# Performance work log

Measured on AMD Instinct MI355X. Metric: run time of the kernel, lower is better.

Reference implementation:

```python
import jax, jax.numpy as jnp
import numpy as np


def _l2norm(x, eps=1e-6):
    # Matches F.normalize(p=2, dim=-1, eps=eps): divide by max(||x||, eps)
    n = jnp.sqrt(jnp.sum(x * x, axis=-1, keepdims=True))
    return x / jnp.maximum(n, eps)


def setup_inputs() -> dict:
    key = jax.random.key(0)
    k0, k1, k2, k3, k4 = jax.random.split(key, 5)
    B, T, H, Dk, Dv = 2, 4096, 16, 128, 128
    q = _l2norm(jax.random.normal(k0, (B, T, H, Dk), dtype=jnp.float32))
    k = _l2norm(jax.random.normal(k1, (B, T, H, Dk), dtype=jnp.float32))
    v = jax.random.normal(k2, (B, T, H, Dv), dtype=jnp.float32)
    # alpha: decay in (0,1) (module: exp(-exp(A_log)*softplus(a+dt_bias)))
    alpha = jax.random.uniform(k3, (B, T, H), dtype=jnp.float32, minval=0.5, maxval=0.999)
    # beta: write gate in (0,1) (module: sigmoid(b))
    beta = jax.random.uniform(k4, (B, T, H), dtype=jnp.float32, minval=0.01, maxval=0.99)
    initial_state = jnp.zeros((B, H, Dk, Dv), dtype=jnp.float32)
    return {"q": q, "k": k, "v": v, "alpha": alpha, "beta": beta,
            "initial_state": initial_state}


def reference(q, k, v, alpha, beta, initial_state):
    """Gated delta rule recurrence (faithful to gdn_recurrent_naive).

    S_t = a_t * (S_{t-1} - b_t * k_t (k_t^T S_{t-1})) + b_t * k_t v_t^T
    o_t = S_t^T q_t
    """
    def step(S, xs):
        q_t, k_t, v_t, a_t, b_t = xs  # (B,H,Dk), (B,H,Dk), (B,H,Dv), (B,H), (B,H)
        a = a_t[..., None, None]
        b = b_t[..., None, None]
        kS = jnp.einsum('bhd,bhdv->bhv', k_t, S)          # k^T S
        S = a * (S - b * jnp.einsum('bhd,bhv->bhdv', k_t, kS)) \
            + b * jnp.einsum('bhd,bhv->bhdv', k_t, v_t)   # delta-rule update
        o = jnp.einsum('bhdv,bhd->bhv', S, q_t)           # read with q
        return S, o

    xs = (q.swapaxes(0, 1), k.swapaxes(0, 1), v.swapaxes(0, 1),
          alpha.swapaxes(0, 1), beta.swapaxes(0, 1))  # time-major for scan
    S_final, outs = jax.lax.scan(step, initial_state.astype(jnp.float32), xs)
    return outs.swapaxes(0, 1), S_final  # (B,T,H,Dv), (B,H,Dk,Dv)
```

## Files before the change

### kernel.cpp

```cpp
#include <hip/hip_runtime.h>

#define T_LEN 4096
#define H_N   16
#define DK    128
#define DV    128
#define LCH   64
#define NCH   64

typedef float f32x4 __attribute__((ext_vector_type(4)));
typedef short s16x8 __attribute__((ext_vector_type(8)));

#define OFF_U0 0
#define OFF_W  32768
#define OFF_Q  49152
#define OFF_KD 65536
#define OFF_G  81920
#define OFF_GM 90112
#define CH_B   90368ull
#define WS_NEED (2048ull * CH_B)

#define SWZ(row) (((row)&7) << 4)

__device__ __forceinline__ unsigned short f2b(float x) {
  unsigned u = __float_as_uint(x);
  return (unsigned short)((u + 0x7FFF + ((u >> 16) & 1)) >> 16);
}

#define GLDS16(gp, lp)                                                        \
  __builtin_amdgcn_global_load_lds(                                           \
      (const __attribute__((address_space(1))) void*)(gp),                    \
      (__attribute__((address_space(3))) void*)(lp), 16, 0, 0)
#define GLDS4(gp, lp)                                                         \
  __builtin_amdgcn_global_load_lds(                                           \
      (const __attribute__((address_space(1))) void*)(gp),                    \
      (__attribute__((address_space(3))) void*)(lp), 4, 0, 0)

#define LBAR()                                                                \
  do {                                                                        \
    asm volatile("s_waitcnt lgkmcnt(0)" ::: "memory");                        \
    __builtin_amdgcn_s_barrier();                                             \
    __builtin_amdgcn_sched_barrier(0);                                        \
  } while (0)

__device__ void solve64(float* RHS, const float* A, int tid) {
#pragma unroll 1
  for (int I = 0; I < 4; ++I) {
    if (I > 0) {
      const int i2 = 16 * I + (tid >> 4), cg = tid & 15;
      float* rp = RHS + i2 * 128 + cg * 8;
      float acc[8];
#pragma unroll
      for (int m = 0; m < 8; ++m) acc[m] = rp[m];
      for (int j = 0; j < 16 * I; ++j) {
        float a = A[i2 * 64 + j];
        const float* yp = RHS + j * 128 + cg * 8;
#pragma unroll
        for (int m = 0; m < 8; ++m) acc[m] = fmaf(-a, yp[m], acc[m]);
      }
#pragma unroll
      for (int m = 0; m < 8; ++m) rp[m] = acc[m];
      __syncthreads();
    }
    if (tid < 128) {
      const int col = tid;
      float y[16];
#pragma unroll
      for (int r = 0; r < 16; ++r) y[r] = RHS[(16 * I + r) * 128 + col];
#pragma unroll
      for (int r = 1; r < 16; ++r) {
        float t = y[r];
#pragma unroll
        for (int j = 0; j < 15; ++j)
          if (j < r) t = fmaf(-A[(16 * I + r) * 64 + 16 * I + j], y[j], t);
        y[r] = t;
      }
#pragma unroll
      for (int r = 0; r < 16; ++r) RHS[(16 * I + r) * 128 + col] = y[r];
    }
    __syncthreads();
  }
}

extern "C" __global__ void __launch_bounds__(256) gdn_p1(
    const float* __restrict__ q, const float* __restrict__ k,
    const float* __restrict__ v, const float* __restrict__ al,
    const float* __restrict__ be, char* __restrict__ ws) {
  __shared__ unsigned char big[32768];
  __shared__ float A_s[64 * 64];
  __shared__ float g_s[64], bb_s[64], sc_s[64];
  unsigned char* Kb = big;
  unsigned char* Qb = big + 16384;
  float* RHS = (float*)big;

  const int bid = blockIdx.x;
  const int bh = bid & 31, c = bid >> 5;
  const int b = bh >> 4, h = bh & 15;
  const int tid = threadIdx.x;
  const int t0 = c * LCH;
  char* wsc = ws + (size_t)(bh * 64 + c) * CH_B;

  if (tid < 64) {
    size_t gi = (size_t)(b * T_LEN + t0 + tid) * H_N + h;
    g_s[tid] = __logf(al[gi]);
    bb_s[tid] = be[gi];
  }
  __syncthreads();
  if (tid == 0) {
    float r = 0.f;
    for (int i = 0; i < 64; ++i) { r += g_s[i]; g_s[i] = r; }
  }
  __syncthreads();
  if (tid < 64) {
    sc_s[tid] = __expf(g_s[tid]);
    *(float*)(wsc + OFF_GM + tid * 4) = sc_s[tid];
  }

  for (int idx = tid; idx < 1024; idx += 256) {
    int row = idx >> 4, grp = idx & 15;
    size_t go = ((size_t)(b * T_LEN + t0 + row) * H_N + h) * DK + grp * 8;
    float4 ka = *(const float4*)(k + go);
    float4 kb2 = *(const float4*)(k + go + 4);
    float4 qa = *(const float4*)(q + go);
    float4 qb2 = *(const float4*)(q + go + 4);
    union { unsigned short u[8]; uint4 v4; } tk, tq;
    tk.u[0] = f2b(ka.x); tk.u[1] = f2b(ka.y); tk.u[2] = f2b(ka.z); tk.u[3] = f2b(ka.w);
    tk.u[4] = f2b(kb2.x); tk.u[5] = f2b(kb2.y); tk.u[6] = f2b(kb2.z); tk.u[7] = f2b(kb2.w);
    tq.u[0] = f2b(qa.x); tq.u[1] = f2b(qa.y); tq.u[2] = f2b(qa.z); tq.u[3] = f2b(qa.w);
    tq.u[4] = f2b(qb2.x); tq.u[5] = f2b(qb2.y); tq.u[6] = f2b(qb2.z); tq.u[7] = f2b(qb2.w);
    int la = (row * 256 + grp * 16) ^ SWZ(row);
    *(uint4*)(Kb + la) = tk.v4;
    *(uint4*)(Qb + la) = tq.v4;
    *(uint4*)(wsc + OFF_Q + la) = tq.v4;
  }
  __syncthreads();

  const int w = tid >> 6, l = tid & 63, li = l & 15, hi = l >> 4;
  f32x4 aK[4], aQ[4];
#pragma unroll
  for (int jt = 0; jt < 4; ++jt) { aK[jt] = (f32x4){0, 0, 0, 0}; aQ[jt] = (f32x4){0, 0, 0, 0}; }
#pragma unroll
  for (int ks = 0; ks < 4; ++ks) {
    int rowA = 16 * w + li;
    int oa = (rowA * 256 + ks * 64 + hi * 16) ^ SWZ(rowA);
    s16x8 fa = *(const s16x8*)(Kb + oa);
    s16x8 fq = *(const s16x8*)(Qb + oa);
#pragma unroll
    for (int jt = 0; jt < 4; ++jt) {
      int rowB = 16 * jt + li;
      s16x8 fb = *(const s16x8*)(Kb + ((rowB * 256 + ks * 64 + hi * 16) ^ SWZ(rowB)));
      aK[jt] = __builtin_amdgcn_mfma_f32_16x16x32_bf16(fa, fb, aK[jt], 0, 0, 0);
      aQ[jt] = __builtin_amdgcn_mfma_f32_16x16x32_bf16(fq, fb, aQ[jt], 0, 0, 0);
    }
  }
#pragma unroll
  for (int jt = 0; jt < 4; ++jt)
#pragma unroll
    for (int r = 0; r < 4; ++r) {
      int i = 16 * w + hi * 4 + r, j = 16 * jt + li;
      float e = __expf(g_s[i] - g_s[j]);
      A_s[i * 64 + j] = (j < i) ? bb_s[i] * e * aK[jt][r] : 0.f;
      *(unsigned short*)(wsc + OFF_G + ((i * 128 + j * 2) ^ SWZ(i))) =
          f2b((j <= i) ? e * aQ[jt][r] : 0.f);
    }
  __syncthreads();

  for (int idx = tid; idx < 2048; idx += 256) {
    int row = idx >> 5, c4 = idx & 31;
    float4 vv = *(const float4*)(v + ((size_t)(b * T_LEN + t0 + row) * H_N + h) * DV + c4 * 4);
    float s = bb_s[row];
    float4 o = {s * vv.x, s * vv.y, s * vv.z, s * vv.w};
    *(float4*)(RHS + row * 128 + c4 * 4) = o;
  }
  __syncthreads();
  solve64(RHS, A_s, tid);
  for (int idx = tid; idx < 2048; idx += 256) {
    int row = idx >> 5, c4 = idx & 31;
    *(float4*)(wsc + OFF_U0 + (c4 >> 2) * 4096 + row * 64 + (c4 & 3) * 16) =
        *(const float4*)(RHS + idx * 4);
  }
  __syncthreads();

  for (int idx = tid; idx < 2048; idx += 256) {
    int row = idx >> 5, c4 = idx & 31;
    float4 kv = *(const float4*)(k + ((size_t)(b * T_LEN + t0 + row) * H_N + h) * DK + c4 * 4);
    float s = bb_s[row] * sc_s[row];
    float4 o = {s * kv.x, s * kv.y, s * kv.z, s * kv.w};
    *(float4*)(RHS + row * 128 + c4 * 4) = o;
  }
  __syncthreads();
  solve64(RHS, A_s, tid);
  for (int idx = tid; idx < 1024; idx += 256) {
    int row = idx >> 4, g8 = idx & 15;
    const float* p = RHS + row * 128 + g8 * 8;
    union { unsigned short u[8]; uint4 v4; } t;
#pragma unroll
    for (int e = 0; e < 8; ++e) t.u[e] = f2b(-p[e]);
    *(uint4*)(wsc + OFF_W + ((row * 256 + g8 * 16) ^ SWZ(row))) = t.v4;
  }
  __syncthreads();

  if (tid < 64) sc_s[tid] = __expf(g_s[63] - g_s[tid]);
  __syncthreads();
  float* Kf = (float*)big;
#pragma unroll 1
  for (int p = 0; p < 2; ++p) {
    for (int idx = tid; idx < 1024; idx += 256) {
      int r = idx >> 5, c4 = idx & 31;
      float4 kv = *(const float4*)(k + ((size_t)(b * T_LEN + t0 + 32 * p + r) * H_N + h) * DK + c4 * 4);
      *(float4*)(Kf + r * 132 + c4 * 4) = kv;
    }
    __syncthreads();
#pragma unroll
    for (int m = 0; m < 16; ++m) {
      int flat = m * 256 + tid;
      int j32 = flat & 31, d = flat >> 5;
      float val = sc_s[32 * p + j32] * Kf[j32 * 132 + d];
      *(unsigned short*)(wsc + OFF_KD + ((d * 128 + (32 * p + j32) * 2) ^ SWZ(d))) = f2b(val);
    }
    __syncthreads();
  }
}

extern "C" __global__ void __launch_bounds__(256, 1) gdn_p2(
    const float* __restrict__ S0, float* __restrict__ out,
    const char* __restrict__ ws) {
  __shared__ unsigned char Wb[2][16384];
  __shared__ unsigned char Qb[2][16384];
  __shared__ unsigned char KDb[2][16384];
  __shared__ unsigned char Gb[2][8192];
  __shared__ float U0s[2][1024];
  __shared__ float gam[2][64];
  __shared__ unsigned char Stb[4096];
  __shared__ unsigned char Ytb[2048];

  const int bid = blockIdx.x;
  const int bh = bid & 31, s = bid >> 5;
  const int b = bh >> 4, h = bh & 15;
  const int tid = threadIdx.x;
  const int w = tid >> 6, lane = tid & 63, li = lane & 15, hi = lane >> 4;
  const char* wsbase = ws + (size_t)bh * 64 * CH_B;

#define STG(CI, P)                                                            \
  do {                                                                        \
    const char* c_ = wsbase + (size_t)(CI) * CH_B;                            \
    _Pragma("unroll") for (int j_ = 0; j_ < 4; ++j_) {                        \
      GLDS16(c_ + OFF_W + j_ * 4096 + tid * 16, &Wb[P][j_ * 4096 + w * 1024]); \
      GLDS16(c_ + OFF_Q + j_ * 4096 + tid * 16, &Qb[P][j_ * 4096 + w * 1024]); \
      GLDS16(c_ + OFF_KD + j_ * 4096 + tid * 16, &KDb[P][j_ * 4096 + w * 1024]); \
    }                                                                         \
    _Pragma("unroll") for (int j_ = 0; j_ < 2; ++j_)                          \
      GLDS16(c_ + OFF_G + j_ * 4096 + tid * 16, &Gb[P][j_ * 4096 + w * 1024]); \
    GLDS16(c_ + OFF_U0 + s * 4096 + tid * 16,                                 \
           (unsigned char*)U0s[P] + w * 1024);                                \
    if (w == 0) GLDS4(c_ + OFF_GM + lane * 4, &gam[P][0]);                    \
  } while (0)

  float S[2][4];
#pragma unroll
  for (int t = 0; t < 2; ++t)
#pragma unroll
    for (int r = 0; r < 4; ++r) {
      int d = (w + 4 * t) * 16 + hi * 4 + r;
      S[t][r] = S0[((size_t)bh * 128 + d) * 128 + s * 16 + li];
    }
#define WRITE_ST()                                                            \
  do {                                                                        \
    _Pragma("unroll") for (int t = 0; t < 2; ++t)                             \
        _Pragma("unroll") for (int r = 0; r < 4; r += 2) {                    \
      int d = (w + 4 * t) * 16 + hi * 4 + r;                                  \
      unsigned pk = (unsigned)f2b(S[t][r]) | ((unsigned)f2b(S[t][r + 1]) << 16); \
      *(unsigned*)(Stb + ((li * 256 + d * 2) ^ SWZ(li))) = pk;                \
    }                                                                         \
  } while (0)

  STG(0, 0);
  WRITE_ST();
  __syncthreads();

#pragma unroll 1
  for (int c = 0; c < NCH; ++c) {
    const int p = c & 1;
    if (c + 1 < NCH) STG(c + 1, p ^ 1);

    s16x8 sfb[4];
#pragma unroll
    for (int ks = 0; ks < 4; ++ks)
      sfb[ks] = *(const s16x8*)(Stb + ((li * 256 + ks * 64 + hi * 16) ^ SWZ(li)));

    f32x4 Y;
#pragma unroll
    for (int r = 0; r < 4; ++r) Y[r] = U0s[p][(16 * w + hi * 4 + r) * 16 + li];
#pragma unroll
    for (int ks = 0; ks < 4; ++ks) {
      s16x8 fa = *(const s16x8*)(Wb[p] + (((16 * w + li) * 256 + ks * 64 + hi * 16) ^ SWZ(li)));
      Y = __builtin_amdgcn_mfma_f32_16x16x32_bf16(fa, sfb[ks], Y, 0, 0, 0);
    }
#pragma unroll
    for (int r = 0; r < 4; r += 2) {
      int j = 16 * w + hi * 4 + r;
      unsigned pk = (unsigned)f2b(Y[r]) | ((unsigned)f2b(Y[r + 1]) << 16);
      *(unsigned*)(Ytb + ((li * 128 + j * 2) ^ SWZ(li))) = pk;
    }
    LBAR();

    f32x4 O = {0, 0, 0, 0};
#pragma unroll
    for (int ks = 0; ks < 4; ++ks) {
      s16x8 fa = *(const s16x8*)(Qb[p] + (((16 * w + li) * 256 + ks * 64 + hi * 16) ^ SWZ(li)));
      O = __builtin_amdgcn_mfma_f32_16x16x32_bf16(fa, sfb[ks], O, 0, 0, 0);
    }
    s16x8 yfb[2];
#pragma unroll
    for (int ks = 0; ks < 2; ++ks)
      yfb[ks] = *(const s16x8*)(Ytb + ((li * 128 + ks * 64 + hi * 16) ^ SWZ(li)));
#pragma unroll
    for (int r = 0; r < 4; ++r) O[r] *= gam[p][16 * w + hi * 4 + r];
#pragma unroll
    for (int ks = 0; ks < 2; ++ks) {
      s16x8 fa = *(const s16x8*)(Gb[p] + (((16 * w + li) * 128 + ks * 64 + hi * 16) ^ SWZ(li)));
      O = __builtin_amdgcn_mfma_f32_16x16x32_bf16(fa, yfb[ks], O, 0, 0, 0);
    }
#pragma unroll
    for (int r = 0; r < 4; ++r) {
      size_t oi = ((size_t)(b * T_LEN + c * 64 + 16 * w + hi * 4 + r) * H_N + h) * DV + s * 16 + li;
      out[oi] = O[r];
    }

    float ge = gam[p][63];
#pragma unroll
    for (int t = 0; t < 2; ++t) {
      f32x4 acc;
#pragma unroll
      for (int r = 0; r < 4; ++r) acc[r] = ge * S[t][r];
#pragma unroll
      for (int ks = 0; ks < 2; ++ks) {
        s16x8 fa = *(const s16x8*)(KDb[p] + ((((w + 4 * t) * 16 + li) * 128 + ks * 64 + hi * 16) ^ SWZ(li)));
        acc = __builtin_amdgcn_mfma_f32_16x16x32_bf16(fa, yfb[ks], acc, 0, 0, 0);
      }
#pragma unroll
      for (int r = 0; r < 4; ++r) S[t][r] = acc[r];
    }
    LBAR();
    WRITE_ST();
    __syncthreads();
  }

#pragma unroll
  for (int t = 0; t < 2; ++t)
#pragma unroll
    for (int r = 0; r < 4; ++r) {
      int d = (w + 4 * t) * 16 + hi * 4 + r;
      out[(size_t)(2 * T_LEN * H_N * DV) + ((size_t)bh * 128 + d) * 128 + s * 16 + li] = S[t][r];
    }
}

#define COLS 16
#define CHUNK 16
#define STEP_B 8192u
#define AB_B 64u
#define OSTRIDE (H_N * DV)
template <int CTRL>
__device__ __forceinline__ float dpp_add(float x) {
  int y = __builtin_amdgcn_update_dpp(0, __float_as_int(x), CTRL, 0xF, 0xF, true);
  return x + __int_as_float(y);
}
__device__ __forceinline__ float red16(float x) {
  x = dpp_add<0xB1>(x); x = dpp_add<0x4E>(x);
  x = dpp_add<0x124>(x); x = dpp_add<0x128>(x);
  return x;
}
extern "C" __global__ void __launch_bounds__(256, 1) gdn_fallback(
    const float* __restrict__ q, const float* __restrict__ k,
    const float* __restrict__ v, const float* __restrict__ al,
    const float* __restrict__ be, const float* __restrict__ S0,
    float* __restrict__ out) {
  __shared__ float kb[2][CHUNK * DK];
  __shared__ float qb[2][CHUNK * DK];
  __shared__ float vb[2][CHUNK * COLS];
  __shared__ float abuf[2][64];
  __shared__ float bbuf[2][64];
  const int bid = blockIdx.x;
  const int bh = bid & 31, g = bid >> 5;
  const int b = bh >> 4, h = bh & 15;
  const int tid = threadIdx.x;
  const int cl = tid >> 4, li = tid & 15, lane = tid & 63, wid = tid >> 6;
  const int col = g * COLS + cl, d0 = li * 8;
  const size_t bh_qk = ((size_t)b * T_LEN * H_N + h) * DK;
  const size_t bh_v = ((size_t)b * T_LEN * H_N + h) * DV;
  const size_t bh_ab = (size_t)b * T_LEN * H_N + h;
  const int fo0 = wid * 2048 + lane * 16, fo1 = fo0 + 1024;
  const char* kg0 = (const char*)(k + bh_qk) + (size_t)(fo0 >> 9) * STEP_B + (fo0 & 511);
  const char* kg1 = (const char*)(k + bh_qk) + (size_t)(fo1 >> 9) * STEP_B + (fo1 & 511);
  const char* qg0 = (const char*)(q + bh_qk) + (size_t)(fo0 >> 9) * STEP_B + (fo0 & 511);
  const char* qg1 = (const char*)(q + bh_qk) + (size_t)(fo1 >> 9) * STEP_B + (fo1 & 511);
  const int fv = lane * 16;
  const char* vg = (const char*)(v + bh_v + g * COLS) + (size_t)(fv >> 6) * STEP_B + (fv & 63);
  const int lcl = lane < 16 ? lane : 15;
  const char* ag = (const char*)(al + bh_ab) + (size_t)lcl * AB_B;
  const char* bg = (const char*)(be + bh_ab) + (size_t)lcl * AB_B;
#define STAGEF(CI, P) do { \
    const size_t off = (size_t)(CI) * (CHUNK * STEP_B); \
    const size_t offab = (size_t)(CI) * (CHUNK * AB_B); \
    GLDS16(kg0 + off, &kb[P][wid * 512]); GLDS16(kg1 + off, &kb[P][wid * 512 + 256]); \
    GLDS16(qg0 + off, &qb[P][wid * 512]); GLDS16(qg1 + off, &qb[P][wid * 512 + 256]); \
    if (wid == 0) GLDS16(vg + off, &vb[P][0]); \
    else if (wid == 1) GLDS4(ag + offab, &abuf[P][0]); \
    else if (wid == 2) GLDS4(bg + offab, &bbuf[P][0]); \
  } while (0)
  float sv[8];
  const float* s0p = S0 + ((size_t)(b * H_N + h) * DK + d0) * DV + col;
#pragma unroll
  for (int j = 0; j < 8; ++j) sv[j] = s0p[(size_t)j * DV];
  STAGEF(0, 0);
  __syncthreads();
  float* op = out + bh_v + col;
  for (int ci = 0; ci < T_LEN / CHUNK; ++ci) {
    const int p = ci & 1;
    if (ci + 1 < T_LEN / CHUNK) STAGEF(ci + 1, p ^ 1);
    const float* kc = kb[p]; const float* qc = qb[p]; const float* vc = vb[p];
    const float* ac = abuf[p]; const float* bc = bbuf[p];
#pragma unroll
    for (int j = 0; j < CHUNK; ++j) {
      f32x4 kA = *(const f32x4*)(kc + j * DK + d0);
      f32x4 kB = *(const f32x4*)(kc + j * DK + d0 + 4);
      f32x4 qA = *(const f32x4*)(qc + j * DK + d0);
      f32x4 qB = *(const f32x4*)(qc + j * DK + d0 + 4);
      float vv = vc[j * COLS + cl], aa = ac[j], bv = bc[j];
      float kk[8] = {kA[0], kA[1], kA[2], kA[3], kB[0], kB[1], kB[2], kB[3]};
      float qq[8] = {qA[0], qA[1], qA[2], qA[3], qB[0], qB[1], qB[2], qB[3]};
      float pk0 = kk[0] * sv[0], pk1 = kk[1] * sv[1];
      float pu0 = qq[0] * sv[0], pu1 = qq[1] * sv[1];
      float pg0 = kk[0] * qq[0], pg1 = kk[1] * qq[1];
#pragma unroll
      for (int m = 2; m < 8; m += 2) {
        pk0 = fmaf(kk[m], sv[m], pk0); pk1 = fmaf(kk[m + 1], sv[m + 1], pk1);
        pu0 = fmaf(qq[m], sv[m], pu0); pu1 = fmaf(qq[m + 1], sv[m + 1], pu1);
        pg0 = fmaf(kk[m], qq[m], pg0); pg1 = fmaf(kk[m + 1], qq[m + 1], pg1);
      }
      float pk = red16(pk0 + pk1), pu = red16(pu0 + pu1), pg = red16(pg0 + pg1);
      float tmp = fmaf(-(bv * aa), pk, bv * vv);
#pragma unroll
      for (int m = 0; m < 8; ++m) sv[m] = fmaf(aa, sv[m], kk[m] * tmp);
      if (li == 0) op[(size_t)(ci * CHUNK + j) * OSTRIDE] = fmaf(pg, tmp, aa * pu);
    }
    __syncthreads();
  }
  float* sf = out + (size_t)2 * T_LEN * H_N * DV + ((size_t)(b * H_N + h) * DK + d0) * DV + col;
#pragma unroll
  for (int j = 0; j < 8; ++j) sf[(size_t)j * DV] = sv[j];
}

extern "C" void kernel_launch(void* const* d_in, const int* in_sizes, int n_in,
                              void* d_out, int out_size, void* d_ws,
                              size_t ws_size, hipStream_t stream) {
  const float* q = (const float*)d_in[0];
  const float* k = (const float*)d_in[1];
  const float* v = (const float*)d_in[2];
  const float* al = (const float*)d_in[3];
  const float* be = (const float*)d_in[4];
  const float* S0 = (const float*)d_in[5];
  float* out = (float*)d_out;

  if (ws_size >= WS_NEED) {
    gdn_p1<<<dim3(2048), dim3(256), 0, stream>>>(q, k, v, al, be, (char*)d_ws);
    gdn_p2<<<dim3(256), dim3(256), 0, stream>>>(S0, out, (const char*)d_ws);
  } else {
    gdn_fallback<<<dim3(256), dim3(256), 0, stream>>>(q, k, v, al, be, S0, out);
  }
}
```

Measured before the change: 296.6 us.

## Solve both triangular systems per-thread in registers, fuse KD write, parallel prefix scan

Replaces the two shared-memory blocked triangular solves with a single register-resident forward substitution. Threads 0-127 each solve one column of the V right-hand side and threads 128-255 each solve one column of the K right-hand side concurrently, with A rows read as float4 from LDS. The serial single-thread cumulative log-decay sum becomes a wavefront shuffle scan, and the decayed-K transpose write is fused into the K load, dropping several barriers and LDS round trips. In exchange each thread holds 64 floats of state, which raises register pressure and may cause spills or lower occupancy, and global loads and stores become strided per column.

```diff
diff --git a/kernel.cpp b/kernel.cpp
--- a/kernel.cpp
+++ b/kernel.cpp
@@ -42,55 +42,15 @@
     __builtin_amdgcn_sched_barrier(0);                                        \
   } while (0)
 
-__device__ void solve64(float* RHS, const float* A, int tid) {
-#pragma unroll 1
-  for (int I = 0; I < 4; ++I) {
-    if (I > 0) {
-      const int i2 = 16 * I + (tid >> 4), cg = tid & 15;
-      float* rp = RHS + i2 * 128 + cg * 8;
-      float acc[8];
-#pragma unroll
-      for (int m = 0; m < 8; ++m) acc[m] = rp[m];
-      for (int j = 0; j < 16 * I; ++j) {
-        float a = A[i2 * 64 + j];
-        const float* yp = RHS + j * 128 + cg * 8;
-#pragma unroll
-        for (int m = 0; m < 8; ++m) acc[m] = fmaf(-a, yp[m], acc[m]);
-      }
-#pragma unroll
-      for (int m = 0; m < 8; ++m) rp[m] = acc[m];
-      __syncthreads();
-    }
-    if (tid < 128) {
-      const int col = tid;
-      float y[16];
-#pragma unroll
-      for (int r = 0; r < 16; ++r) y[r] = RHS[(16 * I + r) * 128 + col];
-#pragma unroll
-      for (int r = 1; r < 16; ++r) {
-        float t = y[r];
-#pragma unroll
-        for (int j = 0; j < 15; ++j)
-          if (j < r) t = fmaf(-A[(16 * I + r) * 64 + 16 * I + j], y[j], t);
-        y[r] = t;
-      }
-#pragma unroll
-      for (int r = 0; r < 16; ++r) RHS[(16 * I + r) * 128 + col] = y[r];
-    }
-    __syncthreads();
-  }
-}
-
 extern "C" __global__ void __launch_bounds__(256) gdn_p1(
     const float* __restrict__ q, const float* __restrict__ k,
     const float* __restrict__ v, const float* __restrict__ al,
     const float* __restrict__ be, char* __restrict__ ws) {
-  __shared__ unsigned char big[32768];
-  __shared__ float A_s[64 * 64];
-  __shared__ float g_s[64], bb_s[64], sc_s[64];
+  __shared__ __align__(16) unsigned char big[32768];
+  __shared__ __align__(16) float A_s[64 * 64];
+  __shared__ float g_s[64], bb_s[64], sc_s[64], rr_s[64], bg_s[64];
   unsigned char* Kb = big;
   unsigned char* Qb = big + 16384;
-  float* RHS = (float*)big;
 
   const int bid = blockIdx.x;
   const int bh = bid & 31, c = bid >> 5;
@@ -101,18 +61,21 @@
 
   if (tid < 64) {
     size_t gi = (size_t)(b * T_LEN + t0 + tid) * H_N + h;
-    g_s[tid] = __logf(al[gi]);
-    bb_s[tid] = be[gi];
-  }
-  __syncthreads();
-  if (tid == 0) {
-    float r = 0.f;
-    for (int i = 0; i < 64; ++i) { r += g_s[i]; g_s[i] = r; }
-  }
-  __syncthreads();
-  if (tid < 64) {
-    sc_s[tid] = __expf(g_s[tid]);
-    *(float*)(wsc + OFF_GM + tid * 4) = sc_s[tid];
+    float x = __logf(al[gi]);
+    float bbv = be[gi];
+#pragma unroll
+    for (int d = 1; d < 64; d <<= 1) {
+      float yv = __shfl_up(x, d, 64);
+      if (tid >= d) x += yv;
+    }
+    float tot = __shfl(x, 63, 64);
+    float gam = __expf(x);
+    g_s[tid] = x;
+    bb_s[tid] = bbv;
+    sc_s[tid] = gam;
+    rr_s[tid] = __expf(tot - x);
+    bg_s[tid] = bbv * gam;
+    *(float*)(wsc + OFF_GM + tid * 4) = gam;
   }
 
   for (int idx = tid; idx < 1024; idx += 256) {
@@ -162,62 +125,82 @@
       *(unsigned short*)(wsc + OFF_G + ((i * 128 + j * 2) ^ SWZ(i))) =
           f2b((j <= i) ? e * aQ[jt][r] : 0.f);
     }
+
+  float y[64];
+  if (tid < 128) {
+    const int cc = tid;
+    const float* vp = v + ((size_t)(b * T_LEN + t0) * H_N + h) * DV + cc;
+#pragma unroll
+    for (int j = 0; j < 64; ++j) y[j] = bb_s[j] * vp[(size_t)j * (H_N * DV)];
+  } else {
+    const int d = tid - 128;
+    const float* kp = k + ((size_t)(b * T_LEN + t0) * H_N + h) * DK + d;
+#pragma unroll
+    for (int m = 0; m < 8; ++m) {
+      float kv[8];
+#pragma unroll
+      for (int e = 0; e < 8; ++e) kv[e] = kp[(size_t)(m * 8 + e) * (H_N * DK)];
+      union { unsigned u2[4]; uint4 v4; } t;
+#pragma unroll
+      for (int e = 0; e < 4; ++e)
+        t.u2[e] = (unsigned)f2b(rr_s[m * 8 + 2 * e] * kv[2 * e]) |
+                  ((unsigned)f2b(rr_s[m * 8 + 2 * e + 1] * kv[2 * e + 1]) << 16);
+      *(uint4*)(wsc + OFF_KD + ((d * 128 + m * 16) ^ SWZ(d))) = t.v4;
+#pragma unroll
+      for (int e = 0; e < 8; ++e) y[m * 8 + e] = bg_s[m * 8 + e] * kv[e];
+    }
+  }
   __syncthreads();
 
-  for (int idx = tid; idx < 2048; idx += 256) {
-    int row = idx >> 5, c4 = idx & 31;
-    float4 vv = *(const float4*)(v + ((size_t)(b * T_LEN + t0 + row) * H_N + h) * DV + c4 * 4);
-    float s = bb_s[row];
-    float4 o = {s * vv.x, s * vv.y, s * vv.z, s * vv.w};
-    *(float4*)(RHS + row * 128 + c4 * 4) = o;
-  }
-  __syncthreads();
-  solve64(RHS, A_s, tid);
-  for (int idx = tid; idx < 2048; idx += 256) {
-    int row = idx >> 5, c4 = idx & 31;
-    *(float4*)(wsc + OFF_U0 + (c4 >> 2) * 4096 + row * 64 + (c4 & 3) * 16) =
-        *(const float4*)(RHS + idx * 4);
-  }
-  __syncthreads();
-
-  for (int idx = tid; idx < 2048; idx += 256) {
-    int row = idx >> 5, c4 = idx & 31;
-    float4 kv = *(const float4*)(k + ((size_t)(b * T_LEN + t0 + row) * H_N + h) * DK + c4 * 4);
-    float s = bb_s[row] * sc_s[row];
-    float4 o = {s * kv.x, s * kv.y, s * kv.z, s * kv.w};
-    *(float4*)(RHS + row * 128 + c4 * 4) = o;
-  }
-  __syncthreads();
-  solve64(RHS, A_s, tid);
-  for (int idx = tid; idx < 1024; idx += 256) {
-    int row = idx >> 4, g8 = idx & 15;
-    const float* p = RHS + row * 128 + g8 * 8;
-    union { unsigned short u[8]; uint4 v4; } t;
-#pragma unroll
-    for (int e = 0; e < 8; ++e) t.u[e] = f2b(-p[e]);
-    *(uint4*)(wsc + OFF_W + ((row * 256 + g8 * 16) ^ SWZ(row))) = t.v4;
-  }
-  __syncthreads();
-
-  if (tid < 64) sc_s[tid] = __expf(g_s[63] - g_s[tid]);
-  __syncthreads();
-  float* Kf = (float*)big;
-#pragma unroll 1
-  for (int p = 0; p < 2; ++p) {
-    for (int idx = tid; idx < 1024; idx += 256) {
-      int r = idx >> 5, c4 = idx & 31;
-      float4 kv = *(const float4*)(k + ((size_t)(b * T_LEN + t0 + 32 * p + r) * H_N + h) * DK + c4 * 4);
-      *(float4*)(Kf + r * 132 + c4 * 4) = kv;
-    }
-    __syncthreads();
-#pragma unroll
-    for (int m = 0; m < 16; ++m) {
-      int flat = m * 256 + tid;
-      int j32 = flat & 31, d = flat >> 5;
-      float val = sc_s[32 * p + j32] * Kf[j32 * 132 + d];
-      *(unsigned short*)(wsc + OFF_KD + ((d * 128 + (32 * p + j32) * 2) ^ SWZ(d))) = f2b(val);
-    }
-    __syncthreads();
+  const float* Af = A_s;
+#pragma unroll
+  for (int I = 0; I < 4; ++I) {
+    if (I > 0) {
+#pragma unroll
+      for (int r = 0; r < 16; ++r) {
+        const int row = 16 * I + r;
+        float a0 = 0.f, a1 = 0.f, a2 = 0.f, a3 = 0.f;
+#pragma unroll
+        for (int j4 = 0; j4 < 4 * I; ++j4) {
+          f32x4 av = *(const f32x4*)(Af + row * 64 + j4 * 4);
+          a0 = fmaf(av[0], y[j4 * 4 + 0], a0);
+          a1 = fmaf(av[1], y[j4 * 4 + 1], a1);
+          a2 = fmaf(av[2], y[j4 * 4 + 2], a2);
+          a3 = fmaf(av[3], y[j4 * 4 + 3], a3);
+        }
+        y[row] -= (a0 + a1) + (a2 + a3);
+      }
+    }
+#pragma unroll
+    for (int r = 1; r < 16; ++r) {
+      const int row = 16 * I + r;
+      float tacc0 = 0.f, tacc1 = 0.f;
+#pragma unroll
+      for (int m = 0; m < (r + 3) / 4; ++m) {
+        f32x4 av = *(const f32x4*)(Af + row * 64 + 16 * I + m * 4);
+#pragma unroll
+        for (int e = 0; e < 4; ++e) {
+          const int j = m * 4 + e;
+          if (j < r) {
+            if (j & 1) tacc1 = fmaf(av[e], y[16 * I + j], tacc1);
+            else       tacc0 = fmaf(av[e], y[16 * I + j], tacc0);
+          }
+        }
+      }
+      y[row] -= tacc0 + tacc1;
+    }
+  }
+
+  if (tid < 128) {
+    const int cc = tid;
+    char* up = wsc + OFF_U0 + (cc >> 4) * 4096 + (cc & 15) * 4;
+#pragma unroll
+    for (int j = 0; j < 64; ++j) *(float*)(up + j * 64) = y[j];
+  } else {
+    const int d = tid - 128;
+#pragma unroll
+    for (int j = 0; j < 64; ++j)
+      *(unsigned short*)(wsc + OFF_W + ((j * 256 + d * 2) ^ SWZ(j))) = f2b(-y[j]);
   }
 }
 
```

After: 670.5 us. +126.1%, slower.
